# Kernel optimization log

Hardware: AMD Instinct MI355X
Metric: run time of the kernel (lower is better)

The kernel has to match this reference:

```python
import jax, jax.numpy as jnp
import numpy as np

WS = 11      # window_size
SIGMA = 1.5
C1 = 0.01 ** 2
C2 = 0.03 ** 2


def _window(channel):
    g = np.exp(-((np.arange(WS) - WS // 2) ** 2) / (2.0 * SIGMA ** 2))
    g = (g / g.sum()).astype(np.float32)
    w2 = np.outer(g, g)  # [WS, WS]
    return jnp.asarray(np.broadcast_to(w2, (channel, 1, WS, WS)).copy())


def _blur(x, w, channel):
    pad = WS // 2
    return jax.lax.conv_general_dilated(
        x, w, window_strides=(1, 1), padding=[(pad, pad), (pad, pad)],
        dimension_numbers=("NCHW", "OIHW", "NCHW"),
        feature_group_count=channel)


def _ssim(img1, img2, w, channel):
    mu1 = _blur(img1, w, channel)
    mu2 = _blur(img2, w, channel)
    mu1_sq = mu1 * mu1
    mu2_sq = mu2 * mu2
    mu1_mu2 = mu1 * mu2
    sigma1_sq = _blur(img1 * img1, w, channel) - mu1_sq
    sigma2_sq = _blur(img2 * img2, w, channel) - mu2_sq
    sigma12 = _blur(img1 * img2, w, channel) - mu1_mu2
    ssim_map = ((2.0 * mu1_mu2 + C1) * (2.0 * sigma12 + C2)) / (
        (mu1_sq + mu2_sq + C1) * (sigma1_sq + sigma2_sq + C2))
    return ssim_map.mean()  # size_average=True


def setup_inputs() -> dict:
    key = jax.random.key(0)
    k1, k2, k3 = jax.random.split(key, 3)
    B, C, H, W = 16, 3, 512, 512
    return {
        "fused_img": jax.random.uniform(k1, (B, C, H, W), dtype=jnp.float32),
        "source_img1": jax.random.uniform(k2, (B, C, H, W), dtype=jnp.float32),
        "source_img2": jax.random.uniform(k3, (B, C, H, W), dtype=jnp.float32),
    }


def reference(fused_img, source_img1, source_img2):
    channel = fused_img.shape[1]
    w = _window(channel).astype(fused_img.dtype)
    ssim1 = _ssim(fused_img, source_img1, w, channel)
    ssim2 = _ssim(fused_img, source_img2, w, channel)
    return 1.0 - (ssim1 + ssim2) / 2.0
```

## Files before the change

kernel.cpp:

```cpp
#include <hip/hip_runtime.h>
#include <cmath>

#define HALO 5
#define TSX 32
#define CH 16
#define CHR 26
#define HSTR 36
#define WIDTH 512
#define HEIGHT 512

struct GW { float g[11]; };

__device__ __forceinline__ float ssim_term(float mu1, float mu2,
                                           float x2b, float y2b, float xyb)
{
    const float C1 = 1e-4f, C2 = 9e-4f;
    float mu12 = mu1 * mu2;
    float num  = (2.f * mu12 + C1) * (2.f * (xyb - mu12) + C2);
    float den  = (mu1 * mu1 + mu2 * mu2 + C1) *
                 ((x2b - mu1 * mu1) + (y2b - mu2 * mu2) + C2);
    return num / den;
}

__global__ __launch_bounds__(256, 5)
void ssim_tile(const float* __restrict__ fI, const float* __restrict__ aI,
               const float* __restrict__ bI, float* __restrict__ bsum,
               GW gw)
{
    __shared__ __align__(16) float hb[8][CHR * HSTR];
    __shared__ float red[4];

    const int tid = threadIdx.x;
    const int x0 = blockIdx.x * TSX;
    const int y0 = blockIdx.y * 32;
    const size_t pbase = (size_t)blockIdx.z * (size_t)(WIDTH * HEIGHT);

    const int rA = tid >> 3;
    const int qA = tid & 7;
    const bool actA = (rA < CHR);
    const int gx0 = x0 + 4 * qA - 8;

    const int jB  = tid & 31;
    const int rgB = tid >> 5;
    const bool actB = (rgB < 4);

    float part = 0.f;

    for (int c = 0; c < 2; ++c) {
        if (c) __syncthreads();
        const int yb = y0 + CH * c - HALO;

        if (actA) {
            const int yy = yb + rA;
            const bool yok = (unsigned)yy < (unsigned)HEIGHT;
            const float* rowf = fI + pbase + (size_t)yy * WIDTH;
            const float* rowa = aI + pbase + (size_t)yy * WIDTH;
            const float* rowb = bI + pbase + (size_t)yy * WIDTH;

            float acc[4][8];
            #pragma unroll
            for (int jj = 0; jj < 4; ++jj)
                #pragma unroll
                for (int q = 0; q < 8; ++q) acc[jj][q] = 0.f;

            #pragma unroll
            for (int k = 0; k < 5; ++k) {
                const int g = gx0 + 4 * k;
                const bool ok = yok && (g >= 0) && (g <= WIDTH - 4);
                float4 vf = ok ? *(const float4*)(rowf + g) : make_float4(0,0,0,0);
                float4 va = ok ? *(const float4*)(rowa + g) : make_float4(0,0,0,0);
                float4 vb = ok ? *(const float4*)(rowb + g) : make_float4(0,0,0,0);
                const float fs[4] = { vf.x, vf.y, vf.z, vf.w };
                const float as[4] = { va.x, va.y, va.z, va.w };
                const float bs[4] = { vb.x, vb.y, vb.z, vb.w };
                #pragma unroll
                for (int cc = 0; cc < 4; ++cc) {
                    const int t = 4 * k + cc - 3;
                    if (t < 0 || t > 13) continue;
                    const float f = fs[cc], a = as[cc], b = bs[cc];
                    float p[8];
                    p[0] = f; p[1] = a; p[2] = b;
                    p[3] = f * f; p[4] = a * a; p[5] = b * b;
                    p[6] = f * a; p[7] = f * b;
                    #pragma unroll
                    for (int jj = 0; jj < 4; ++jj) {
                        const int u = t - jj;
                        if (u >= 0 && u <= 10) {
                            const float w = gw.g[u];
                            #pragma unroll
                            for (int q = 0; q < 8; ++q)
                                acc[jj][q] = fmaf(w, p[q], acc[jj][q]);
                        }
                    }
                }
            }
            #pragma unroll
            for (int q = 0; q < 8; ++q) {
                *(float4*)(&hb[q][rA * HSTR + 4 * qA]) =
                    make_float4(acc[0][q], acc[1][q], acc[2][q], acc[3][q]);
            }
        }
        __syncthreads();

        if (actB) {
            const int R = 4 * rgB;
            float acc2[4][8];
            #pragma unroll
            for (int ri = 0; ri < 4; ++ri)
                #pragma unroll
                for (int q = 0; q < 8; ++q) acc2[ri][q] = 0.f;
            #pragma unroll
            for (int k = 0; k < 14; ++k) {
                float hv[8];
                #pragma unroll
                for (int q = 0; q < 8; ++q)
                    hv[q] = hb[q][(R + k) * HSTR + jB];
                #pragma unroll
                for (int ri = 0; ri < 4; ++ri) {
                    const int u = k - ri;
                    if (u >= 0 && u <= 10) {
                        const float w = gw.g[u];
                        #pragma unroll
                        for (int q = 0; q < 8; ++q)
                            acc2[ri][q] = fmaf(w, hv[q], acc2[ri][q]);
                    }
                }
            }
            #pragma unroll
            for (int ri = 0; ri < 4; ++ri) {
                part += ssim_term(acc2[ri][0], acc2[ri][1],
                                  acc2[ri][3], acc2[ri][4], acc2[ri][6]);
                part += ssim_term(acc2[ri][0], acc2[ri][2],
                                  acc2[ri][3], acc2[ri][5], acc2[ri][7]);
            }
        }
    }

    #pragma unroll
    for (int off = 32; off > 0; off >>= 1) part += __shfl_down(part, off);
    if ((tid & 63) == 0) red[tid >> 6] = part;
    __syncthreads();
    if (tid == 0) {
        int bid = blockIdx.x + gridDim.x * (blockIdx.y + gridDim.y * blockIdx.z);
        bsum[bid] = red[0] + red[1] + red[2] + red[3];
    }
}

__global__ __launch_bounds__(256)
void ssim_final(const float* __restrict__ bsum, float* __restrict__ out,
                int nb, float invTwoN)
{
    __shared__ float sred[4];
    float s = 0.f;
    for (int i = threadIdx.x; i < nb; i += 256) s += bsum[i];
    #pragma unroll
    for (int off = 32; off > 0; off >>= 1) s += __shfl_down(s, off);
    if ((threadIdx.x & 63) == 0) sred[threadIdx.x >> 6] = s;
    __syncthreads();
    if (threadIdx.x == 0)
        out[0] = 1.f - (sred[0] + sred[1] + sred[2] + sred[3]) * invTwoN;
}

extern "C" void kernel_launch(void* const* d_in, const int* in_sizes, int n_in,
                              void* d_out, int out_size, void* d_ws, size_t ws_size,
                              hipStream_t stream)
{
    const float* f  = (const float*)d_in[0];
    const float* s1 = (const float*)d_in[1];
    const float* s2 = (const float*)d_in[2];
    float* out  = (float*)d_out;
    float* bsum = (float*)d_ws;

    const int N = in_sizes[0];
    const int planes = N / (WIDTH * HEIGHT);

    GW gw;
    double gd[11], gs = 0.0;
    for (int i = 0; i < 11; ++i) {
        double d = (double)(i - 5);
        gd[i] = exp(-(d * d) / 4.5);
        gs += gd[i];
    }
    for (int i = 0; i < 11; ++i) gw.g[i] = (float)(gd[i] / gs);

    dim3 grid(WIDTH / TSX, HEIGHT / 32, planes);
    const int nb = (WIDTH / TSX) * (HEIGHT / 32) * planes;
    ssim_tile<<<grid, dim3(256), 0, stream>>>(f, s1, s2, bsum, gw);
    ssim_final<<<1, dim3(256), 0, stream>>>(bsum, out, nb, 0.5f / (float)N);
}
```

Baseline: 265.5 us.

## Use ring-buffered horizontal pass over taller tiles and specialize interior blocks

The tile height doubles to 64 rows and is processed in four 16-row chunks. A 26-row ring buffer in shared memory keeps the 10 halo rows of horizontal-blur results between chunks, so overlapping rows are not reloaded or recomputed. Interior blocks use a template variant with no bounds checks, and the final SSIM division becomes a hardware reciprocal. The cost is halved block count, which means less parallelism, some extra modulo index arithmetic, and a small precision change from the approximate reciprocal.

```diff
diff --git a/kernel.cpp b/kernel.cpp
--- a/kernel.cpp
+++ b/kernel.cpp
@@ -3,56 +3,55 @@
 
 #define HALO 5
 #define TSX 32
+#define TILE_H 64
+#define NCHUNK 4
 #define CH 16
-#define CHR 26
+#define RING 26
 #define HSTR 36
+#define PLANE (RING * HSTR)
 #define WIDTH 512
 #define HEIGHT 512
 
 struct GW { float g[11]; };
 
-__device__ __forceinline__ float ssim_term(float mu1, float mu2,
-                                           float x2b, float y2b, float xyb)
+__device__ __forceinline__ float ssim2(float mu1, float mu2,
+                                       float x2b, float y2b, float xyb)
 {
     const float C1 = 1e-4f, C2 = 9e-4f;
     float mu12 = mu1 * mu2;
     float num  = (2.f * mu12 + C1) * (2.f * (xyb - mu12) + C2);
     float den  = (mu1 * mu1 + mu2 * mu2 + C1) *
                  ((x2b - mu1 * mu1) + (y2b - mu2 * mu2) + C2);
-    return num / den;
-}
-
-__global__ __launch_bounds__(256, 5)
-void ssim_tile(const float* __restrict__ fI, const float* __restrict__ aI,
-               const float* __restrict__ bI, float* __restrict__ bsum,
-               GW gw)
-{
-    __shared__ __align__(16) float hb[8][CHR * HSTR];
-    __shared__ float red[4];
-
-    const int tid = threadIdx.x;
-    const int x0 = blockIdx.x * TSX;
-    const int y0 = blockIdx.y * 32;
-    const size_t pbase = (size_t)blockIdx.z * (size_t)(WIDTH * HEIGHT);
-
-    const int rA = tid >> 3;
-    const int qA = tid & 7;
-    const bool actA = (rA < CHR);
+    return num * __builtin_amdgcn_rcpf(den);
+}
+
+template<bool CHK>
+__device__ __forceinline__ float tile_compute(
+    const float* __restrict__ fI, const float* __restrict__ aI,
+    const float* __restrict__ bI, float (* __restrict__ hb)[PLANE],
+    const GW& gw, int tid, int x0, int y0, size_t pbase)
+{
+    const int rA  = tid >> 3;
+    const int qA  = tid & 7;
     const int gx0 = x0 + 4 * qA - 8;
-
     const int jB  = tid & 31;
     const int rgB = tid >> 5;
     const bool actB = (rgB < 4);
 
     float part = 0.f;
 
-    for (int c = 0; c < 2; ++c) {
+    #pragma unroll 1
+    for (int c = 0; c < NCHUNK; ++c) {
         if (c) __syncthreads();
-        const int yb = y0 + CH * c - HALO;
-
-        if (actA) {
-            const int yy = yb + rA;
-            const bool yok = (unsigned)yy < (unsigned)HEIGHT;
+
+        const int nA = c ? CH : RING;
+        if (rA < nA) {
+            const int t = c ? (16 * c + 10 + rA) : rA;
+            int slot = t;
+            slot -= (slot >= RING) ? RING : 0;
+            slot -= (slot >= RING) ? RING : 0;
+            const int yy = y0 - HALO + t;
+            const bool yok = CHK ? ((unsigned)yy < (unsigned)HEIGHT) : true;
             const float* rowf = fI + pbase + (size_t)yy * WIDTH;
             const float* rowa = aI + pbase + (size_t)yy * WIDTH;
             const float* rowb = bI + pbase + (size_t)yy * WIDTH;
@@ -66,17 +65,24 @@
             #pragma unroll
             for (int k = 0; k < 5; ++k) {
                 const int g = gx0 + 4 * k;
-                const bool ok = yok && (g >= 0) && (g <= WIDTH - 4);
-                float4 vf = ok ? *(const float4*)(rowf + g) : make_float4(0,0,0,0);
-                float4 va = ok ? *(const float4*)(rowa + g) : make_float4(0,0,0,0);
-                float4 vb = ok ? *(const float4*)(rowb + g) : make_float4(0,0,0,0);
+                float4 vf, va, vb;
+                if (CHK) {
+                    const bool ok = yok && ((unsigned)g <= (unsigned)(WIDTH - 4));
+                    vf = ok ? *(const float4*)(rowf + g) : make_float4(0,0,0,0);
+                    va = ok ? *(const float4*)(rowa + g) : make_float4(0,0,0,0);
+                    vb = ok ? *(const float4*)(rowb + g) : make_float4(0,0,0,0);
+                } else {
+                    vf = *(const float4*)(rowf + g);
+                    va = *(const float4*)(rowa + g);
+                    vb = *(const float4*)(rowb + g);
+                }
                 const float fs[4] = { vf.x, vf.y, vf.z, vf.w };
                 const float as[4] = { va.x, va.y, va.z, va.w };
                 const float bs[4] = { vb.x, vb.y, vb.z, vb.w };
                 #pragma unroll
                 for (int cc = 0; cc < 4; ++cc) {
-                    const int t = 4 * k + cc - 3;
-                    if (t < 0 || t > 13) continue;
+                    const int tt = 4 * k + cc - 3;
+                    if (tt < 0 || tt > 13) continue;
                     const float f = fs[cc], a = as[cc], b = bs[cc];
                     float p[8];
                     p[0] = f; p[1] = a; p[2] = b;
@@ -84,7 +90,7 @@
                     p[6] = f * a; p[7] = f * b;
                     #pragma unroll
                     for (int jj = 0; jj < 4; ++jj) {
-                        const int u = t - jj;
+                        const int u = tt - jj;
                         if (u >= 0 && u <= 10) {
                             const float w = gw.g[u];
                             #pragma unroll
@@ -95,15 +101,16 @@
                 }
             }
             #pragma unroll
-            for (int q = 0; q < 8; ++q) {
-                *(float4*)(&hb[q][rA * HSTR + 4 * qA]) =
+            for (int q = 0; q < 8; ++q)
+                *(float4*)(&hb[q][slot * HSTR + 4 * qA]) =
                     make_float4(acc[0][q], acc[1][q], acc[2][q], acc[3][q]);
-            }
         }
         __syncthreads();
 
         if (actB) {
-            const int R = 4 * rgB;
+            int sb = 16 * c + 4 * rgB;
+            sb -= (sb >= RING) ? RING : 0;
+            sb -= (sb >= RING) ? RING : 0;
             float acc2[4][8];
             #pragma unroll
             for (int ri = 0; ri < 4; ++ri)
@@ -111,10 +118,12 @@
                 for (int q = 0; q < 8; ++q) acc2[ri][q] = 0.f;
             #pragma unroll
             for (int k = 0; k < 14; ++k) {
+                int s = sb + k;
+                s -= (s >= RING) ? RING : 0;
+                const float* hp = &hb[0][s * HSTR + jB];
                 float hv[8];
                 #pragma unroll
-                for (int q = 0; q < 8; ++q)
-                    hv[q] = hb[q][(R + k) * HSTR + jB];
+                for (int q = 0; q < 8; ++q) hv[q] = hp[q * PLANE];
                 #pragma unroll
                 for (int ri = 0; ri < 4; ++ri) {
                     const int u = k - ri;
@@ -128,13 +137,35 @@
             }
             #pragma unroll
             for (int ri = 0; ri < 4; ++ri) {
-                part += ssim_term(acc2[ri][0], acc2[ri][1],
-                                  acc2[ri][3], acc2[ri][4], acc2[ri][6]);
-                part += ssim_term(acc2[ri][0], acc2[ri][2],
-                                  acc2[ri][3], acc2[ri][5], acc2[ri][7]);
+                part += ssim2(acc2[ri][0], acc2[ri][1],
+                              acc2[ri][3], acc2[ri][4], acc2[ri][6]);
+                part += ssim2(acc2[ri][0], acc2[ri][2],
+                              acc2[ri][3], acc2[ri][5], acc2[ri][7]);
             }
         }
     }
+    return part;
+}
+
+__global__ __launch_bounds__(256, 5)
+void ssim_tile(const float* __restrict__ fI, const float* __restrict__ aI,
+               const float* __restrict__ bI, float* __restrict__ bsum,
+               GW gw)
+{
+    __shared__ __align__(16) float hb[8][PLANE];
+    __shared__ float red[4];
+
+    const int tid = threadIdx.x;
+    const int x0 = blockIdx.x * TSX;
+    const int y0 = blockIdx.y * TILE_H;
+    const size_t pbase = (size_t)blockIdx.z * (size_t)(WIDTH * HEIGHT);
+
+    const bool interior = (blockIdx.x > 0) && (blockIdx.x < gridDim.x - 1) &&
+                          (blockIdx.y > 0) && (blockIdx.y < gridDim.y - 1);
+
+    float part = interior
+        ? tile_compute<false>(fI, aI, bI, hb, gw, tid, x0, y0, pbase)
+        : tile_compute<true >(fI, aI, bI, hb, gw, tid, x0, y0, pbase);
 
     #pragma unroll
     for (int off = 32; off > 0; off >>= 1) part += __shfl_down(part, off);
@@ -183,8 +214,8 @@
     }
     for (int i = 0; i < 11; ++i) gw.g[i] = (float)(gd[i] / gs);
 
-    dim3 grid(WIDTH / TSX, HEIGHT / 32, planes);
-    const int nb = (WIDTH / TSX) * (HEIGHT / 32) * planes;
+    dim3 grid(WIDTH / TSX, HEIGHT / TILE_H, planes);
+    const int nb = (WIDTH / TSX) * (HEIGHT / TILE_H) * planes;
     ssim_tile<<<grid, dim3(256), 0, stream>>>(f, s1, s2, bsum, gw);
     ssim_final<<<1, dim3(256), 0, stream>>>(bsum, out, nb, 0.5f / (float)N);
 }
```

New measurement: 248.2 us. 6.5% less time.
